# Kernel optimization log

Hardware: AMD Instinct MI355X
Metric: run time of the kernel (lower is better)

Reference implementation:

```python
import jax, jax.numpy as jnp
import numpy as np

L, H, HS, D, T, V, B = 6, 6, 64, 384, 256, 65, 64
EPS = 1e-5


def layer_norm(x, g, b):
    m = x.mean(-1, keepdims=True)
    v = x.var(-1, keepdims=True)
    return (x - m) / jnp.sqrt(v + EPS) * g + b


def setup_inputs() -> dict:
    key = jax.random.key(0)
    ks = jax.random.split(key, 12)
    s = 0.02
    return {
        "idx": jax.random.randint(ks[0], (B, T), 0, V),
        "targets": jax.random.randint(ks[1], (B, T), 0, V),
        "tok_emb": s * jax.random.normal(ks[2], (V, D), jnp.float32),
        "pos_emb": s * jax.random.normal(ks[3], (T, D), jnp.float32),
        "Wq": s * jax.random.normal(ks[4], (L, H, D, HS), jnp.float32),
        "Wk": s * jax.random.normal(ks[5], (L, H, D, HS), jnp.float32),
        "Wv": s * jax.random.normal(ks[6], (L, H, D, HS), jnp.float32),
        "Wproj": s * jax.random.normal(ks[7], (L, D, D), jnp.float32),
        "bproj": jnp.zeros((L, D), jnp.float32),
        "W1": s * jax.random.normal(ks[8], (L, D, 4 * D), jnp.float32),
        "b1": jnp.zeros((L, 4 * D), jnp.float32),
        "W2": s * jax.random.normal(ks[9], (L, 4 * D, D), jnp.float32),
        "b2": jnp.zeros((L, D), jnp.float32),
        "ln1_g": jnp.ones((L, D), jnp.float32),
        "ln1_b": jnp.zeros((L, D), jnp.float32),
        "lnf_g": jnp.ones((D,), jnp.float32),
        "lnf_b": jnp.zeros((D,), jnp.float32),
        "Whead": s * jax.random.normal(ks[10], (D, V), jnp.float32),
        "bhead": jnp.zeros((V,), jnp.float32),
    }


def reference(idx, targets, tok_emb, pos_emb, Wq, Wk, Wv, Wproj, bproj,
              W1, b1, W2, b2, ln1_g, ln1_b, lnf_g, lnf_b, Whead, bhead):
    b, t = idx.shape
    x = tok_emb[idx] + pos_emb[:t]  # [B,T,D]
    mask = jnp.tril(jnp.ones((t, t), bool))
    scale = x.shape[-1] ** -0.5  # NOTE: original scales by n_emb_d**-0.5, not head_size**-0.5
    for l in range(L):
        y = layer_norm(x, ln1_g[l], ln1_b[l])
        q = jnp.einsum('btd,hde->bhte', y, Wq[l])
        k = jnp.einsum('btd,hde->bhte', y, Wk[l])
        v = jnp.einsum('btd,hde->bhte', y, Wv[l])
        w = jnp.einsum('bhte,bhse->bhts', q, k) * scale
        w = jnp.where(mask, w, -jnp.inf)
        w = jax.nn.softmax(w, axis=-1)
        o = jnp.einsum('bhts,bhse->bhte', w, v)
        o = o.transpose(0, 2, 1, 3).reshape(b, t, H * HS)  # concat heads on last dim
        x = x + o @ Wproj[l] + bproj[l]
        # NOTE: original Block reuses ln1 (not ln2) before the FFN -- replicated faithfully
        y2 = layer_norm(x, ln1_g[l], ln1_b[l])
        x = x + jax.nn.relu(y2 @ W1[l] + b1[l]) @ W2[l] + b2[l]
    x = layer_norm(x, lnf_g, lnf_b)
    logits = x @ Whead + bhead  # [B,T,V]
    logp = jax.nn.log_softmax(logits, axis=-1)
    loss = -jnp.take_along_axis(logp, targets[..., None], axis=-1).mean()
    return logits, loss
```

## Files before the change

### kernel.cpp

```cpp
#include <hip/hip_runtime.h>
#include <math.h>

#define L_ 6
#define H_ 6
#define HS_ 64
#define D_ 384
#define T_ 256
#define V_ 65
#define B_ 64
#define ROWS (B_*T_)
#define QKVN 1152
#define EPS_ 1e-5f

typedef __attribute__((ext_vector_type(8))) __bf16 bf16x8;
typedef __attribute__((ext_vector_type(2))) __bf16 bf16x2;
typedef __attribute__((ext_vector_type(4))) float f32x4;

__device__ __forceinline__ bf16x8 u4_to_bf8(uint4 u) {
    return __builtin_bit_cast(bf16x8, u);
}

__device__ __forceinline__ void glds16(const void* g, void* l) {
    __builtin_amdgcn_global_load_lds(
        (const __attribute__((address_space(1))) void*)g,
        (__attribute__((address_space(3))) void*)l, 16, 0, 0);
}

__global__ __launch_bounds__(256)
void embed_kernel(const int* __restrict__ idx,
                  const float* __restrict__ tok,
                  const float* __restrict__ pos,
                  float* __restrict__ x) {
    int i = blockIdx.x * blockDim.x + threadIdx.x;
    int e = i * 4;
    int d = e % D_;
    int row = e / D_;
    int t = row % T_;
    const float4 tv = *(const float4*)(tok + (size_t)idx[row]*D_ + d);
    const float4 pv = *(const float4*)(pos + (size_t)t*D_ + d);
    float4 r;
    r.x = tv.x + pv.x; r.y = tv.y + pv.y;
    r.z = tv.z + pv.z; r.w = tv.w + pv.w;
    *(float4*)(x + e) = r;
}

__global__ __launch_bounds__(256)
void ln4(const float* __restrict__ x,
         const float* __restrict__ g,
         const float* __restrict__ b,
         __bf16* __restrict__ yb) {
    int w = threadIdx.x >> 6, lane = threadIdx.x & 63;
    int row = blockIdx.x * 4 + w;
    const float* xr = x + (size_t)row * D_;
    float2 v[3];
    #pragma unroll
    for (int i = 0; i < 3; ++i) v[i] = *(const float2*)(xr + lane*2 + 128*i);
    float s = 0.f, sq = 0.f;
    #pragma unroll
    for (int i = 0; i < 3; ++i) {
        s += v[i].x + v[i].y;
        sq += v[i].x*v[i].x + v[i].y*v[i].y;
    }
    for (int off = 32; off; off >>= 1) {
        s  += __shfl_xor(s,  off);
        sq += __shfl_xor(sq, off);
    }
    float mean = s * (1.0f/D_);
    float var  = sq * (1.0f/D_) - mean*mean;
    float rstd = rsqrtf(var + EPS_);
    __bf16* yr = yb + (size_t)row * D_;
    #pragma unroll
    for (int i = 0; i < 3; ++i) {
        int c = lane*2 + 128*i;
        float2 gv = *(const float2*)(g + c);
        float2 bv = *(const float2*)(b + c);
        bf16x2 pr;
        pr[0] = (__bf16)((v[i].x-mean)*rstd*gv.x + bv.x);
        pr[1] = (__bf16)((v[i].y-mean)*rstd*gv.y + bv.y);
        *(bf16x2*)(yr + c) = pr;
    }
}

__global__ __launch_bounds__(256)
void transpose_cast(const float* __restrict__ src, __bf16* __restrict__ dst,
                    int R, int C, int zdiv, long sA, long sB, long dbase)
{
    __shared__ float tile[32][33];
    int z = blockIdx.z;
    const float* s = src + (long)z * R * C;
    __bf16* d = dst + dbase + (long)(z / zdiv) * sA + (long)(z % zdiv) * sB;
    int c0 = blockIdx.x * 32, r0 = blockIdx.y * 32;
    int t = threadIdx.x;
    int tr = t >> 3, tc = (t & 7) * 4;
    float4 v = *(const float4*)(s + (long)(r0 + tr) * C + c0 + tc);
    tile[tr][tc+0] = v.x; tile[tr][tc+1] = v.y;
    tile[tr][tc+2] = v.z; tile[tr][tc+3] = v.w;
    __syncthreads();
    #pragma unroll
    for (int j = 0; j < 4; ++j)
        d[(long)(c0 + tr) * R + r0 + tc + j] = (__bf16)tile[tc+j][tr];
}

__global__ __launch_bounds__(256)
void head_prep(const float* __restrict__ Whead, __bf16* __restrict__ headT) {
    int i = blockIdx.x * 256 + threadIdx.x;
    int n = i / D_, k = i % D_;
    headT[i] = (n < V_) ? (__bf16)Whead[k*V_ + n] : (__bf16)0.0f;
}

__global__ __launch_bounds__(256)
void gemm64b(const __bf16* __restrict__ A, const __bf16* __restrict__ Bt,
             const float* __restrict__ bias, const float* res,
             float* outF, __bf16* outB,
             int K, int ldc, int ncols, int relu)
{
    __shared__ __align__(16) __bf16 As[2][64*64];
    __shared__ __align__(16) __bf16 Bs[2][128*64];
    int t = threadIdx.x;
    int w = t >> 6, lane = t & 63;
    int ln = lane & 15, quad = lane >> 4;
    int m0 = blockIdx.x * 64, n0 = blockIdx.y * 128;
    int wm = (w >> 1) * 32, wn = (w & 1) * 64;

    f32x4 acc[2][4] = {};

    const char* Ab = (const char*)A + (size_t)m0 * K * 2;
    const char* Bb = (const char*)Bt + (size_t)n0 * K * 2;
    int fb = w*64 + lane;
    size_t gaA[2]; int loA[2];
    #pragma unroll
    for (int ra = 0; ra < 2; ++ra) {
        int f = fb + 256*ra;
        gaA[ra] = (size_t)(f >> 3) * (K*2) + (size_t)(((f & 7) ^ ((f >> 3) & 7)) * 16);
        loA[ra] = (w*64 + 256*ra) * 16;
    }
    size_t gaB[4]; int loB[4];
    #pragma unroll
    for (int rb = 0; rb < 4; ++rb) {
        int f = fb + 256*rb;
        gaB[rb] = (size_t)(f >> 3) * (K*2) + (size_t)(((f & 7) ^ ((f >> 3) & 7)) * 16);
        loB[rb] = (w*64 + 256*rb) * 16;
    }

    int nIt = K >> 6;

    #define STAGE64B(buf, itv) do {                                        \
        size_t kb_ = (size_t)(itv) * 128;                                  \
        _Pragma("unroll")                                                  \
        for (int ra = 0; ra < 2; ++ra)                                     \
            glds16(Ab + gaA[ra] + kb_, (char*)As[buf] + loA[ra]);          \
        _Pragma("unroll")                                                  \
        for (int rb = 0; rb < 4; ++rb)                                     \
            glds16(Bb + gaB[rb] + kb_, (char*)Bs[buf] + loB[rb]);          \
    } while (0)

    STAGE64B(0, 0);

    for (int it = 0; it < nIt; ++it) {
        int p = it & 1;
        __syncthreads();
        if (it + 1 < nIt)
            STAGE64B(p^1, it + 1);
        bf16x8 af[2][2], bfr[4][2];
        #pragma unroll
        for (int i = 0; i < 2; ++i) {
            int row = wm + i*16 + ln;
            #pragma unroll
            for (int kk = 0; kk < 2; ++kk)
                af[i][kk] = __builtin_bit_cast(bf16x8,
                    *(const uint4*)&As[p][row*64 + (((kk*4 + quad) ^ (row & 7)) * 8)]);
        }
        #pragma unroll
        for (int j = 0; j < 4; ++j) {
            int row = wn + j*16 + ln;
            #pragma unroll
            for (int kk = 0; kk < 2; ++kk)
                bfr[j][kk] = __builtin_bit_cast(bf16x8,
                    *(const uint4*)&Bs[p][row*64 + (((kk*4 + quad) ^ (row & 7)) * 8)]);
        }
        #pragma unroll
        for (int kk = 0; kk < 2; ++kk)
            #pragma unroll
            for (int i = 0; i < 2; ++i)
                #pragma unroll
                for (int j = 0; j < 4; ++j)
                    acc[i][j] = __builtin_amdgcn_mfma_f32_16x16x32_bf16(
                                    af[i][kk], bfr[j][kk], acc[i][j], 0, 0, 0);
    }
    #undef STAGE64B

    #pragma unroll
    for (int i = 0; i < 2; ++i) {
        #pragma unroll
        for (int r = 0; r < 4; ++r) {
            int row = m0 + wm + i*16 + quad*4 + r;
            #pragma unroll
            for (int j = 0; j < 4; ++j) {
                int col = n0 + wn + j*16 + ln;
                if (col < ncols) {
                    float v = acc[i][j][r];
                    if (bias) v += bias[col];
                    if (relu) v = fmaxf(v, 0.f);
                    if (res)  v += res[(size_t)row*ldc + col];
                    if (outF) outF[(size_t)row*ldc + col] = v;
                    if (outB) outB[(size_t)row*ldc + col] = (__bf16)v;
                }
            }
        }
    }
}

__global__ __launch_bounds__(256)
void gemm128b(const __bf16* __restrict__ A, const __bf16* __restrict__ Bt,
              const float* __restrict__ bias,
              float* outF, __bf16* outB,
              int K, int ldc, int ncols, int relu)
{
    __shared__ __align__(16) __bf16 As[2][128*64];
    __shared__ __align__(16) __bf16 Bs[2][128*64];
    int t = threadIdx.x;
    int w = t >> 6, lane = t & 63;
    int ln = lane & 15, quad = lane >> 4;
    int m0 = blockIdx.x * 128, n0 = blockIdx.y * 128;
    int wm = (w >> 1) * 64, wn = (w & 1) * 64;

    f32x4 acc[4][4] = {};

    const char* Ab = (const char*)A + (size_t)m0 * K * 2;
    const char* Bb = (const char*)Bt + (size_t)n0 * K * 2;
    int fb = w*64 + lane;
    size_t gaA[4]; int loA[4];
    #pragma unroll
    for (int ra = 0; ra < 4; ++ra) {
        int f = fb + 256*ra;
        gaA[ra] = (size_t)(f >> 3) * (K*2) + (size_t)(((f & 7) ^ ((f >> 3) & 7)) * 16);
        loA[ra] = (w*64 + 256*ra) * 16;
    }
    size_t gaB[4]; int loB[4];
    #pragma unroll
    for (int rb = 0; rb < 4; ++rb) {
        int f = fb + 256*rb;
        gaB[rb] = (size_t)(f >> 3) * (K*2) + (size_t)(((f & 7) ^ ((f >> 3) & 7)) * 16);
        loB[rb] = (w*64 + 256*rb) * 16;
    }

    int nIt = K >> 6;

    #define STAGE128B(buf, itv) do {                                       \
        size_t kb_ = (size_t)(itv) * 128;                                  \
        _Pragma("unroll")                                                  \
        for (int ra = 0; ra < 4; ++ra)                                     \
            glds16(Ab + gaA[ra] + kb_, (char*)As[buf] + loA[ra]);          \
        _Pragma("unroll")                                                  \
        for (int rb = 0; rb < 4; ++rb)                                     \
            glds16(Bb + gaB[rb] + kb_, (char*)Bs[buf] + loB[rb]);          \
    } while (0)

    STAGE128B(0, 0);

    for (int it = 0; it < nIt; ++it) {
        int p = it & 1;
        __syncthreads();
        if (it + 1 < nIt)
            STAGE128B(p^1, it + 1);
        bf16x8 af[4][2], bfr[4][2];
        #pragma unroll
        for (int i = 0; i < 4; ++i) {
            int row = wm + i*16 + ln;
            #pragma unroll
            for (int kk = 0; kk < 2; ++kk)
                af[i][kk] = __builtin_bit_cast(bf16x8,
                    *(const uint4*)&As[p][row*64 + (((kk*4 + quad) ^ (row & 7)) * 8)]);
        }
        #pragma unroll
        for (int j = 0; j < 4; ++j) {
            int row = wn + j*16 + ln;
            #pragma unroll
            for (int kk = 0; kk < 2; ++kk)
                bfr[j][kk] = __builtin_bit_cast(bf16x8,
                    *(const uint4*)&Bs[p][row*64 + (((kk*4 + quad) ^ (row & 7)) * 8)]);
        }
        #pragma unroll
        for (int kk = 0; kk < 2; ++kk)
            #pragma unroll
            for (int i = 0; i < 4; ++i)
                #pragma unroll
                for (int j = 0; j < 4; ++j)
                    acc[i][j] = __builtin_amdgcn_mfma_f32_16x16x32_bf16(
                                    af[i][kk], bfr[j][kk], acc[i][j], 0, 0, 0);
    }
    #undef STAGE128B

    #pragma unroll
    for (int i = 0; i < 4; ++i) {
        #pragma unroll
        for (int r = 0; r < 4; ++r) {
            int row = m0 + wm + i*16 + quad*4 + r;
            #pragma unroll
            for (int j = 0; j < 4; ++j) {
                int col = n0 + wn + j*16 + ln;
                if (col < ncols) {
                    float v = acc[i][j][r];
                    if (bias) v += bias[col];
                    if (relu) v = fmaxf(v, 0.f);
                    if (outF) outF[(size_t)row*ldc + col] = v;
                    if (outB) outB[(size_t)row*ldc + col] = (__bf16)v;
                }
            }
        }
    }
}

__global__ __launch_bounds__(256, 2)
void attn4(const __bf16* __restrict__ qkv, __bf16* __restrict__ o)
{
    __shared__ __align__(16) __bf16 Ks[256*72];
    __shared__ __align__(16) __bf16 Vt[64*264];
    __shared__ __align__(16) __bf16 Pw[4][32*40];
    int bid = blockIdx.x;
    int h = bid % H_;
    int b = bid / H_;
    int t = threadIdx.x;
    int w = t >> 6, lane = t & 63;
    int ln = lane & 15, quad = lane >> 4;
    const size_t rowb = (size_t)b * T_ * QKVN;
    const int hoff = h * HS_;
    const float scale = 0.05103103630798288f;

    for (int c = t; c < 2048; c += 256) {
        int r = c >> 3, e0 = (c & 7) * 8;
        uint4 uk = *(const uint4*)(qkv + rowb + (size_t)r*QKVN + 384 + hoff + e0);
        *(uint4*)&Ks[r*72 + e0] = uk;
        uint4 uv = *(const uint4*)(qkv + rowb + (size_t)r*QKVN + 768 + hoff + e0);
        bf16x8 v8 = u4_to_bf8(uv);
        #pragma unroll
        for (int j = 0; j < 8; ++j) {
            int e = e0 + j;
            Vt[e*264 + (((r >> 3) ^ ((e >> 3) & 3)) * 8) + (r & 7)] = v8[j];
        }
    }

    int qis[2] = { w, 7 - w };
    uint4 Qf[2][2][2];
    #pragma unroll
    for (int tl = 0; tl < 2; ++tl)
        #pragma unroll
        for (int mi = 0; mi < 2; ++mi)
            #pragma unroll
            for (int kc = 0; kc < 2; ++kc)
                Qf[tl][mi][kc] = *(const uint4*)(qkv + rowb +
                    (size_t)(qis[tl]*32 + mi*16 + ln)*QKVN + hoff + kc*32 + quad*8);

    __syncthreads();

    __bf16* P = Pw[w];
    #pragma unroll
    for (int tl = 0; tl < 2; ++tl) {
        int qi = qis[tl];
        f32x4 O[2][4] = {};
        float mst[2][4], lst[2][4];
        #pragma unroll
        for (int mi = 0; mi < 2; ++mi)
            #pragma unroll
            for (int r = 0; r < 4; ++r) { mst[mi][r] = -INFINITY; lst[mi][r] = 0.f; }

        for (int st = 0; st <= qi; ++st) {
            int sb = st * 32;
            f32x4 S[2][2] = {};
            #pragma unroll
            for (int kc = 0; kc < 2; ++kc) {
                uint4 Kf[2];
                #pragma unroll
                for (int ji = 0; ji < 2; ++ji)
                    Kf[ji] = *(const uint4*)&Ks[(sb + ji*16 + ln)*72 + kc*32 + quad*8];
                __builtin_amdgcn_s_setprio(1);
                #pragma unroll
                for (int mi = 0; mi < 2; ++mi) {
                    bf16x8 qa = __builtin_bit_cast(bf16x8, Qf[tl][mi][kc]);
                    #pragma unroll
                    for (int ji = 0; ji < 2; ++ji)
                        S[mi][ji] = __builtin_amdgcn_mfma_f32_16x16x32_bf16(
                            qa, __builtin_bit_cast(bf16x8, Kf[ji]), S[mi][ji], 0, 0, 0);
                }
                __builtin_amdgcn_s_setprio(0);
            }
            int diag = (st == qi);
            #pragma unroll
            for (int mi = 0; mi < 2; ++mi)
                #pragma unroll
                for (int ji = 0; ji < 2; ++ji)
                    #pragma unroll
                    for (int r = 0; r < 4; ++r) {
                        float v = S[mi][ji][r] * scale;
                        if (diag && (ji*16 + ln) > (mi*16 + quad*4 + r)) v = -INFINITY;
                        S[mi][ji][r] = v;
                    }
            #pragma unroll
            for (int mi = 0; mi < 2; ++mi)
                #pragma unroll
                for (int r = 0; r < 4; ++r) {
                    float mx = fmaxf(S[mi][0][r], S[mi][1][r]);
                    #pragma unroll
                    for (int off = 1; off < 16; off <<= 1)
                        mx = fmaxf(mx, __shfl_xor(mx, off));
                    float mn = fmaxf(mst[mi][r], mx);
                    float al = __expf(mst[mi][r] - mn);
                    mst[mi][r] = mn;
                    float p0 = __expf(S[mi][0][r] - mn);
                    float p1 = __expf(S[mi][1][r] - mn);
                    S[mi][0][r] = p0; S[mi][1][r] = p1;
                    float rs = p0 + p1;
                    #pragma unroll
                    for (int off = 1; off < 16; off <<= 1)
                        rs += __shfl_xor(rs, off);
                    lst[mi][r] = lst[mi][r]*al + rs;
                    #pragma unroll
                    for (int ei = 0; ei < 4; ++ei) O[mi][ei][r] *= al;
                }
            #pragma unroll
            for (int mi = 0; mi < 2; ++mi)
                #pragma unroll
                for (int ji = 0; ji < 2; ++ji)
                    #pragma unroll
                    for (int r = 0; r < 4; ++r)
                        P[(mi*16 + quad*4 + r)*40 + ji*16 + ln] = (__bf16)S[mi][ji][r];
            uint4 Pf[2], Vf[4];
            #pragma unroll
            for (int mi = 0; mi < 2; ++mi)
                Pf[mi] = *(const uint4*)&P[(mi*16 + ln)*40 + quad*8];
            #pragma unroll
            for (int ei = 0; ei < 4; ++ei) {
                int e = ei*16 + ln;
                Vf[ei] = *(const uint4*)&Vt[e*264 + (((st*4 + quad) ^ ((e >> 3) & 3)) * 8)];
            }
            __builtin_amdgcn_s_setprio(1);
            #pragma unroll
            for (int mi = 0; mi < 2; ++mi)
                #pragma unroll
                for (int ei = 0; ei < 4; ++ei)
                    O[mi][ei] = __builtin_amdgcn_mfma_f32_16x16x32_bf16(
                        __builtin_bit_cast(bf16x8, Pf[mi]),
                        __builtin_bit_cast(bf16x8, Vf[ei]), O[mi][ei], 0, 0, 0);
            __builtin_amdgcn_s_setprio(0);
        }
        #pragma unroll
        for (int mi = 0; mi < 2; ++mi)
            #pragma unroll
            for (int r = 0; r < 4; ++r) {
                float inv = 1.0f / lst[mi][r];
                size_t row = (size_t)(b*T_ + qi*32 + mi*16 + quad*4 + r);
                #pragma unroll
                for (int ei = 0; ei < 4; ++ei)
                    o[row*D_ + hoff + ei*16 + ln] = (__bf16)(O[mi][ei][r] * inv);
            }
    }
}

__global__ __launch_bounds__(256)
void loss2(const float* __restrict__ logits,
           const int* __restrict__ tg,
           float* __restrict__ loss)
{
    int t = threadIdx.x;
    int g16 = t >> 4, ln = t & 15;
    int row = blockIdx.x * 16 + g16;
    const float* lr = logits + (size_t)row * V_;
    float v0 = lr[ln], v1 = lr[16+ln], v2 = lr[32+ln], v3 = lr[48+ln];
    float v4 = (ln == 0) ? lr[64] : -INFINITY;
    float m = fmaxf(fmaxf(fmaxf(v0, v1), fmaxf(v2, v3)), v4);
    #pragma unroll
    for (int off = 1; off < 16; off <<= 1) m = fmaxf(m, __shfl_xor(m, off));
    float s = __expf(v0-m) + __expf(v1-m) + __expf(v2-m) + __expf(v3-m);
    if (ln == 0) s += __expf(v4-m);
    #pragma unroll
    for (int off = 1; off < 16; off <<= 1) s += __shfl_xor(s, off);
    float val = 0.f;
    if (ln == 0)
        val = -(lr[tg[row]] - m - __logf(s)) * (1.0f/ROWS);
    #pragma unroll
    for (int off = 16; off < 64; off <<= 1) val += __shfl_xor(val, off);
    __shared__ float red[4];
    int w = t >> 6;
    if ((t & 63) == 0) red[w] = val;
    __syncthreads();
    if (t == 0)
        atomicAdd(loss, red[0]+red[1]+red[2]+red[3]);
}

extern "C" void kernel_launch(void* const* d_in, const int* in_sizes, int n_in,
                              void* d_out, int out_size, void* d_ws, size_t ws_size,
                              hipStream_t stream)
{
    const int*   idx     = (const int*)  d_in[0];
    const int*   targets = (const int*)  d_in[1];
    const float* tok     = (const float*)d_in[2];
    const float* pos     = (const float*)d_in[3];
    const float* Wq      = (const float*)d_in[4];
    const float* Wk      = (const float*)d_in[5];
    const float* Wv      = (const float*)d_in[6];
    const float* Wproj   = (const float*)d_in[7];
    const float* bproj   = (const float*)d_in[8];
    const float* W1      = (const float*)d_in[9];
    const float* b1      = (const float*)d_in[10];
    const float* W2      = (const float*)d_in[11];
    const float* b2      = (const float*)d_in[12];
    const float* ln1g    = (const float*)d_in[13];
    const float* ln1b    = (const float*)d_in[14];
    const float* lnfg    = (const float*)d_in[15];
    const float* lnfb    = (const float*)d_in[16];
    const float* Whead   = (const float*)d_in[17];
    const float* bhead   = (const float*)d_in[18];

    float* logits = (float*)d_out;
    float* loss   = logits + (size_t)ROWS * V_;

    const size_t SZ = (size_t)ROWS * D_;
    const size_t RGELEMS = (size_t)ROWS * 4 * D_;

    float*  x   = (float*)d_ws;
    __bf16* yb  = (__bf16*)(x + SZ);
    __bf16* Rg  = yb + SZ;
    __bf16* qkv = Rg;
    __bf16* hid = Rg;
    __bf16* o   = Rg + RGELEMS;
    __bf16* qkvT  = o + SZ;
    __bf16* projT = qkvT + (size_t)L_*QKVN*D_;
    __bf16* w1T   = projT + (size_t)L_*D_*D_;
    __bf16* w2T   = w1T + (size_t)L_*D_*4*D_;
    __bf16* headT = w2T + (size_t)L_*D_*4*D_;

    transpose_cast<<<dim3(2,12,36),256,0,stream>>>(Wq, qkvT, D_, HS_, H_,
        (long)QKVN*D_, (long)HS_*D_, 0L);
    transpose_cast<<<dim3(2,12,36),256,0,stream>>>(Wk, qkvT, D_, HS_, H_,
        (long)QKVN*D_, (long)HS_*D_, (long)D_*D_);
    transpose_cast<<<dim3(2,12,36),256,0,stream>>>(Wv, qkvT, D_, HS_, H_,
        (long)QKVN*D_, (long)HS_*D_, 2L*D_*D_);
    transpose_cast<<<dim3(12,12,6),256,0,stream>>>(Wproj, projT, D_, D_, 1,
        (long)D_*D_, 0L, 0L);
    transpose_cast<<<dim3(48,12,6),256,0,stream>>>(W1, w1T, D_, 4*D_, 1,
        (long)D_*4*D_, 0L, 0L);
    transpose_cast<<<dim3(12,48,6),256,0,stream>>>(W2, w2T, 4*D_, D_, 1,
        (long)D_*4*D_, 0L, 0L);
    head_prep<<<(128*D_)/256, 256, 0, stream>>>(Whead, headT);

    embed_kernel<<<(ROWS*D_/4)/256, 256, 0, stream>>>(idx, tok, pos, x);

    for (int l = 0; l < L_; ++l) {
        ln4<<<ROWS/4, 256, 0, stream>>>(x, ln1g + l*D_, ln1b + l*D_, yb);
        gemm128b<<<dim3(ROWS/128, QKVN/128), 256, 0, stream>>>(
            yb, qkvT + (size_t)l*QKVN*D_, nullptr, nullptr, qkv,
            D_, QKVN, QKVN, 0);
        attn4<<<B_*H_, 256, 0, stream>>>(qkv, o);
        gemm64b<<<dim3(ROWS/64, D_/128), 256, 0, stream>>>(
            o, projT + (size_t)l*D_*D_, bproj + l*D_, x, x, nullptr,
            D_, D_, D_, 0);
        ln4<<<ROWS/4, 256, 0, stream>>>(x, ln1g + l*D_, ln1b + l*D_, yb);
        gemm128b<<<dim3(ROWS/128, 4*D_/128), 256, 0, stream>>>(
            yb, w1T + (size_t)l*D_*4*D_, b1 + l*4*D_, nullptr, hid,
            D_, 4*D_, 4*D_, 1);
        gemm64b<<<dim3(ROWS/64, D_/128), 256, 0, stream>>>(
            hid, w2T + (size_t)l*D_*4*D_, b2 + l*D_, x, x, nullptr,
            4*D_, D_, D_, 0);
    }
    ln4<<<ROWS/4, 256, 0, stream>>>(x, lnfg, lnfb, yb);
    gemm64b<<<dim3(ROWS/64, 1), 256, 0, stream>>>(
        yb, headT, bhead, nullptr, logits, nullptr,
        D_, V_, V_, 0);
    hipMemsetAsync(loss, 0, sizeof(float), stream);
    loss2<<<ROWS/16, 256, 0, stream>>>(logits, targets, loss);
}
```

Baseline: 1.446 ms.

## Single-buffer 128x128 GEMM LDS to raise occupancy

Replaces the double-buffered LDS staging in the 128x128 bf16 GEMM with a single buffer, loading each K-tile and then synchronizing before and after compute. LDS per block drops from 64KB to 32KB, and launch bounds request 3 blocks per CU so more wavefronts can hide latency. In exchange, the prefetch overlap of the next tile's global-to-LDS load with the current MFMA work is lost, and an extra barrier is added per iteration.

```diff
diff --git a/kernel.cpp b/kernel.cpp
--- a/kernel.cpp
+++ b/kernel.cpp
@@ -210,14 +210,14 @@
     }
 }
 
-__global__ __launch_bounds__(256)
-void gemm128b(const __bf16* __restrict__ A, const __bf16* __restrict__ Bt,
+__global__ __launch_bounds__(256, 3)
+void gemm128s(const __bf16* __restrict__ A, const __bf16* __restrict__ Bt,
               const float* __restrict__ bias,
               float* outF, __bf16* outB,
               int K, int ldc, int ncols, int relu)
 {
-    __shared__ __align__(16) __bf16 As[2][128*64];
-    __shared__ __align__(16) __bf16 Bs[2][128*64];
+    __shared__ __align__(16) __bf16 As[128*64];
+    __shared__ __align__(16) __bf16 Bs[128*64];
     int t = threadIdx.x;
     int w = t >> 6, lane = t & 63;
     int ln = lane & 15, quad = lane >> 4;
@@ -246,23 +246,15 @@
 
     int nIt = K >> 6;
 
-    #define STAGE128B(buf, itv) do {                                       \
-        size_t kb_ = (size_t)(itv) * 128;                                  \
-        _Pragma("unroll")                                                  \
-        for (int ra = 0; ra < 4; ++ra)                                     \
-            glds16(Ab + gaA[ra] + kb_, (char*)As[buf] + loA[ra]);          \
-        _Pragma("unroll")                                                  \
-        for (int rb = 0; rb < 4; ++rb)                                     \
-            glds16(Bb + gaB[rb] + kb_, (char*)Bs[buf] + loB[rb]);          \
-    } while (0)
-
-    STAGE128B(0, 0);
-
     for (int it = 0; it < nIt; ++it) {
-        int p = it & 1;
+        size_t kb = (size_t)it * 128;
+        #pragma unroll
+        for (int ra = 0; ra < 4; ++ra)
+            glds16(Ab + gaA[ra] + kb, (char*)As + loA[ra]);
+        #pragma unroll
+        for (int rb = 0; rb < 4; ++rb)
+            glds16(Bb + gaB[rb] + kb, (char*)Bs + loB[rb]);
         __syncthreads();
-        if (it + 1 < nIt)
-            STAGE128B(p^1, it + 1);
         bf16x8 af[4][2], bfr[4][2];
         #pragma unroll
         for (int i = 0; i < 4; ++i) {
@@ -270,7 +262,7 @@
             #pragma unroll
             for (int kk = 0; kk < 2; ++kk)
                 af[i][kk] = __builtin_bit_cast(bf16x8,
-                    *(const uint4*)&As[p][row*64 + (((kk*4 + quad) ^ (row & 7)) * 8)]);
+                    *(const uint4*)&As[row*64 + (((kk*4 + quad) ^ (row & 7)) * 8)]);
         }
         #pragma unroll
         for (int j = 0; j < 4; ++j) {
@@ -278,7 +270,7 @@
             #pragma unroll
             for (int kk = 0; kk < 2; ++kk)
                 bfr[j][kk] = __builtin_bit_cast(bf16x8,
-                    *(const uint4*)&Bs[p][row*64 + (((kk*4 + quad) ^ (row & 7)) * 8)]);
+                    *(const uint4*)&Bs[row*64 + (((kk*4 + quad) ^ (row & 7)) * 8)]);
         }
         #pragma unroll
         for (int kk = 0; kk < 2; ++kk)
@@ -288,8 +280,8 @@
                 for (int j = 0; j < 4; ++j)
                     acc[i][j] = __builtin_amdgcn_mfma_f32_16x16x32_bf16(
                                     af[i][kk], bfr[j][kk], acc[i][j], 0, 0, 0);
-    }
-    #undef STAGE128B
+        __syncthreads();
+    }
 
     #pragma unroll
     for (int i = 0; i < 4; ++i) {
@@ -547,7 +539,7 @@
 
     for (int l = 0; l < L_; ++l) {
         ln4<<<ROWS/4, 256, 0, stream>>>(x, ln1g + l*D_, ln1b + l*D_, yb);
-        gemm128b<<<dim3(ROWS/128, QKVN/128), 256, 0, stream>>>(
+        gemm128s<<<dim3(ROWS/128, QKVN/128), 256, 0, stream>>>(
             yb, qkvT + (size_t)l*QKVN*D_, nullptr, nullptr, qkv,
             D_, QKVN, QKVN, 0);
         attn4<<<B_*H_, 256, 0, stream>>>(qkv, o);
@@ -555,7 +547,7 @@
             o, projT + (size_t)l*D_*D_, bproj + l*D_, x, x, nullptr,
             D_, D_, D_, 0);
         ln4<<<ROWS/4, 256, 0, stream>>>(x, ln1g + l*D_, ln1b + l*D_, yb);
-        gemm128b<<<dim3(ROWS/128, 4*D_/128), 256, 0, stream>>>(
+        gemm128s<<<dim3(ROWS/128, 4*D_/128), 256, 0, stream>>>(
             yb, w1T + (size_t)l*D_*4*D_, b1 + l*4*D_, nullptr, hid,
             D_, 4*D_, 4*D_, 1);
         gemm64b<<<dim3(ROWS/64, D_/128), 256, 0, stream>>>(
```

Result: faster. 1.323 ms (-8.5%).
